# Kernel tuning notes

Measured on AMD Instinct MI355X. Metric: run time of the kernel, lower is better.

Reference implementation:

```python
import jax, jax.numpy as jnp
import numpy as np

NUM_SUBSET = 3
BN_EPS = 1e-5


def setup_inputs() -> dict:
    key = jax.random.key(0)
    ks = jax.random.split(key, 6)
    N, C, T, V = 32, 192, 256, 25
    x = jax.random.normal(ks[0], (N, C, T, V), dtype=jnp.float32)
    w_in = jax.random.normal(ks[1], (3 * C, C), dtype=jnp.float32) * (1.0 / np.sqrt(C))
    b_in = jax.random.normal(ks[2], (3 * C,), dtype=jnp.float32) * 0.02
    w_ff = jax.random.normal(ks[3], (C, C), dtype=jnp.float32) * (1.0 / np.sqrt(C))
    b_ff = jax.random.normal(ks[4], (C,), dtype=jnp.float32) * 0.02
    bn_gamma = jnp.ones((C,), dtype=jnp.float32)
    bn_beta = jnp.zeros((C,), dtype=jnp.float32)
    bn_mean = jnp.zeros((C,), dtype=jnp.float32)
    bn_var = jnp.ones((C,), dtype=jnp.float32)
    return dict(x=x, w_in=w_in, b_in=b_in, w_ff=w_ff, b_ff=b_ff,
                bn_gamma=bn_gamma, bn_beta=bn_beta, bn_mean=bn_mean, bn_var=bn_var)


def reference(x, w_in, b_in, w_ff, b_ff, bn_gamma, bn_beta, bn_mean, bn_var):
    N, C, T, V = x.shape
    S = NUM_SUBSET
    mid = C // S
    # 1x1 conv QKV projection: (N,C,T,V) x (3C,C) -> (N,3C,T,V)
    qkv = jnp.einsum('nctv,dc->ndtv', x, w_in) + b_in[None, :, None, None]
    qkv = qkv.reshape(N, 3 * S, mid, T, V)
    q, k, v = jnp.split(qkv, 3, axis=1)  # each (N,S,mid,T,V)
    # tanh-normalized attention over time: (N,S,T,T)
    att = jnp.tanh(jnp.einsum('nsctv,nscqv->nstq', q, k) / (mid * V))
    y = jnp.einsum('nstq,nscqv->nsctv', att, v).reshape(N, C, T, V)
    # ff_nett: 1x1 conv + BatchNorm (inference form)
    y = jnp.einsum('nctv,dc->ndtv', y, w_ff) + b_ff[None, :, None, None]
    inv = bn_gamma / jnp.sqrt(bn_var + BN_EPS)
    y = (y - bn_mean[None, :, None, None]) * inv[None, :, None, None] + bn_beta[None, :, None, None]
    # residual + LeakyReLU(0.1)
    z = x + y
    return jnp.where(z >= 0, z, 0.1 * z)
```

## Files before the change

kernel.cpp:

```cpp
#include <hip/hip_runtime.h>

#define TV 6400
#define NCH 192
#define D3 576

typedef unsigned short u16;
typedef unsigned int   u32;

typedef __attribute__((ext_vector_type(8))) short bf16x8;
typedef __attribute__((ext_vector_type(4))) float f32x4;

__device__ __forceinline__ float bf2f(u32 h) { return __uint_as_float(h << 16); }
__device__ __forceinline__ u16 f2bf(float f) {
    u32 u = __float_as_uint(f);
    return (u16)((u + 0x7FFFu + ((u >> 16) & 1u)) >> 16);
}

__global__ __launch_bounds__(256) void k_wcast(const float* __restrict__ w_in,
                                               const float* __restrict__ w_ff,
                                               u32* __restrict__ wb) {
    int i = blockIdx.x * 256 + threadIdx.x;
    float2 f;
    if (i < 55296) f = *(const float2*)(w_in + 2 * i);
    else           f = *(const float2*)(w_ff + 2 * (i - 55296));
    wb[i] = (u32)f2bf(f.x) | ((u32)f2bf(f.y) << 16);
}

__global__ __launch_bounds__(256) void k_qkv(const float* __restrict__ x,
                                             const u16* __restrict__ w_inb,
                                             const float* __restrict__ b_in,
                                             u16* __restrict__ qkv,
                                             u16* __restrict__ qt,
                                             u16* __restrict__ kt) {
    const int p0 = blockIdx.x * 128, n = blockIdx.y;
    const int tid = threadIdx.x;
    const int wid = tid >> 6, lane = tid & 63;
    const int wd = wid & 1, wp = wid >> 1;
    const int ml = lane & 15, kq = lane >> 4;

    __shared__ __align__(16) char Bs[128 * 384];
    __shared__ __align__(16) char As[64 * 384];
    float* L = (float*)As;

    for (int cc = 0; cc < 6; ++cc) {
        const float* xn = x + ((size_t)n * NCH + cc * 32) * TV + p0;
#pragma unroll
        for (int r = 0; r < 4; ++r) {
            int idx = tid + 256 * r;
            int c = idx >> 5, p4 = idx & 31;
            float4 v = *(const float4*)(xn + (size_t)c * TV + p4 * 4);
            *(float4*)&L[c * 129 + p4 * 4] = v;
        }
        __syncthreads();
        {
            int p = tid >> 1, half = tid & 1;
            u32 buf[8];
#pragma unroll
            for (int j = 0; j < 8; ++j) {
                float f0 = L[(half * 16 + 2 * j) * 129 + p];
                float f1 = L[(half * 16 + 2 * j + 1) * 129 + p];
                buf[j] = (u32)f2bf(f0) | ((u32)f2bf(f1) << 16);
            }
#pragma unroll
            for (int h = 0; h < 2; ++h) {
                int g = cc * 4 + half * 2 + h;
                uint4 u;
                u.x = buf[h * 4]; u.y = buf[h * 4 + 1];
                u.z = buf[h * 4 + 2]; u.w = buf[h * 4 + 3];
                *(uint4*)(Bs + p * 384 + (((g & ~7) | ((g ^ p) & 7)) << 4)) = u;
            }
        }
        __syncthreads();
    }

    for (int dt = 0; dt < 9; ++dt) {
#pragma unroll
        for (int r = 0; r < 6; ++r) {
            int idx = tid + 256 * r;
            int row = idx / 24, g = idx - row * 24;
            uint4 v = *(const uint4*)(w_inb + (size_t)(dt * 64 + row) * 192 + g * 8);
            *(uint4*)(As + row * 384 + (((g & ~7) | ((g ^ row) & 7)) << 4)) = v;
        }
        __syncthreads();

        bf16x8 aw[2][3][2];
#pragma unroll
        for (int mt = 0; mt < 2; ++mt) {
            int row = wd * 32 + mt * 16 + ml;
#pragma unroll
            for (int kk = 0; kk < 3; ++kk)
#pragma unroll
                for (int ks = 0; ks < 2; ++ks) {
                    int g = kk * 8 + ks * 4 + kq;
                    aw[mt][kk][ks] = *(const bf16x8*)(As + row * 384 + (((g & ~7) | ((g ^ row) & 7)) << 4));
                }
        }

        f32x4 acc[2][4];
#pragma unroll
        for (int i = 0; i < 2; i++)
#pragma unroll
            for (int j = 0; j < 4; j++)
#pragma unroll
                for (int r = 0; r < 4; r++) acc[i][j][r] = 0.f;

#pragma unroll
        for (int kk = 0; kk < 3; ++kk)
#pragma unroll
            for (int ks = 0; ks < 2; ++ks) {
                int g = kk * 8 + ks * 4 + kq;
                bf16x8 bx[4];
#pragma unroll
                for (int nt = 0; nt < 4; ++nt) {
                    int row = wp * 64 + nt * 16 + ml;
                    bx[nt] = *(const bf16x8*)(Bs + row * 384 + (((g & ~7) | ((g ^ row) & 7)) << 4));
                }
#pragma unroll
                for (int mt = 0; mt < 2; ++mt)
#pragma unroll
                    for (int nt = 0; nt < 4; ++nt)
                        acc[mt][nt] = __builtin_amdgcn_mfma_f32_16x16x32_bf16(aw[mt][kk][ks], bx[nt], acc[mt][nt], 0, 0, 0);
            }

        if (dt < 6) {
            const int s = (dt < 3) ? dt : dt - 3;
            u16* dstb = (dt < 3 ? qt : kt) + ((size_t)(n * 3 + s) * 6400 + p0) * 64;
#pragma unroll
            for (int mt = 0; mt < 2; ++mt) {
                int c = wd * 32 + mt * 16 + kq * 4;
                float4 bias = *(const float4*)(b_in + dt * 64 + c);
#pragma unroll
                for (int nt = 0; nt < 4; ++nt) {
                    int p = wp * 64 + nt * 16 + ml;
                    u32 w0 = (u32)f2bf(acc[mt][nt][0] + bias.x) | ((u32)f2bf(acc[mt][nt][1] + bias.y) << 16);
                    u32 w1 = (u32)f2bf(acc[mt][nt][2] + bias.z) | ((u32)f2bf(acc[mt][nt][3] + bias.w) << 16);
                    uint2 u; u.x = w0; u.y = w1;
                    *(uint2*)(dstb + (size_t)p * 64 + c) = u;
                }
            }
        } else {
#pragma unroll
            for (int mt = 0; mt < 2; ++mt) {
                int d = dt * 64 + wd * 32 + mt * 16 + kq * 4;
                float4 bias = *(const float4*)(b_in + d);
                u16* vdst = qkv + ((size_t)n * D3 + d) * TV;
#pragma unroll
                for (int nt = 0; nt < 4; ++nt) {
                    int p = p0 + wp * 64 + nt * 16 + ml;
                    vdst[(size_t)0 * TV + p] = f2bf(acc[mt][nt][0] + bias.x);
                    vdst[(size_t)1 * TV + p] = f2bf(acc[mt][nt][1] + bias.y);
                    vdst[(size_t)2 * TV + p] = f2bf(acc[mt][nt][2] + bias.z);
                    vdst[(size_t)3 * TV + p] = f2bf(acc[mt][nt][3] + bias.w);
                }
            }
        }
        __syncthreads();
    }
}

__global__ __launch_bounds__(256) void k_scores(const u16* __restrict__ qt,
                                                const u16* __restrict__ kt,
                                                u16* __restrict__ att) {
    const int b = blockIdx.z, t0 = blockIdx.y * 128, q0 = blockIdx.x * 128;
    const int tid = threadIdx.x;
    const int wid = tid >> 6, lane = tid & 63;
    const int wm = wid & 1, wn = wid >> 1;
    const int ml = lane & 15, kq = lane >> 4;

    __shared__ __align__(16) char As[128 * 128];
    __shared__ __align__(16) char Bs[128 * 128];

    f32x4 acc[4][4];
#pragma unroll
    for (int i = 0; i < 4; i++)
#pragma unroll
        for (int j = 0; j < 4; j++)
#pragma unroll
            for (int r = 0; r < 4; r++) acc[i][j][r] = 0.f;

    const u16* qb = qt + (size_t)b * 256 * 1600;
    const u16* kb = kt + (size_t)b * 256 * 1600;

    for (int kc = 0; kc < 1600; kc += 64) {
#pragma unroll
        for (int r = 0; r < 4; r++) {
            int idx = tid + 256 * r;
            int row = idx >> 3, g = idx & 7;
            uint4 v = *(const uint4*)(qb + (size_t)(t0 + row) * 1600 + kc + g * 8);
            *(uint4*)(As + row * 128 + (((g ^ row) & 7) << 4)) = v;
        }
#pragma unroll
        for (int r = 0; r < 4; r++) {
            int idx = tid + 256 * r;
            int row = idx >> 3, g = idx & 7;
            uint4 v = *(const uint4*)(kb + (size_t)(q0 + row) * 1600 + kc + g * 8);
            *(uint4*)(Bs + row * 128 + (((g ^ row) & 7) << 4)) = v;
        }
        __syncthreads();
#pragma unroll
        for (int ks = 0; ks < 2; ks++) {
            int gb = ks * 4 + kq;
            bf16x8 a[4], bb[4];
#pragma unroll
            for (int mt = 0; mt < 4; mt++) {
                int row = wm * 64 + mt * 16 + ml;
                a[mt] = *(const bf16x8*)(As + row * 128 + (((gb ^ row) & 7) << 4));
            }
#pragma unroll
            for (int nt = 0; nt < 4; nt++) {
                int row = wn * 64 + nt * 16 + ml;
                bb[nt] = *(const bf16x8*)(Bs + row * 128 + (((gb ^ row) & 7) << 4));
            }
#pragma unroll
            for (int mt = 0; mt < 4; mt++)
#pragma unroll
                for (int nt = 0; nt < 4; nt++)
                    acc[mt][nt] = __builtin_amdgcn_mfma_f32_16x16x32_bf16(a[mt], bb[nt], acc[mt][nt], 0, 0, 0);
        }
        __syncthreads();
    }

    const float sc = 1.0f / 1600.0f;
    u16* ab = att + (size_t)b * 65536;
#pragma unroll
    for (int mt = 0; mt < 4; mt++)
#pragma unroll
        for (int nt = 0; nt < 4; nt++) {
            int q = q0 + wn * 64 + nt * 16 + ml;
#pragma unroll
            for (int r = 0; r < 4; r++) {
                int t = t0 + wm * 64 + mt * 16 + kq * 4 + r;
                ab[(size_t)t * 256 + q] = f2bf(tanhf(acc[mt][nt][r] * sc));
            }
        }
}

__global__ __launch_bounds__(256) void k_trv(const u16* __restrict__ qkv,
                                             u16* __restrict__ vt) {
    const int q0 = blockIdx.x * 32;
    const int c0 = blockIdx.y * 32;
    const int b  = blockIdx.z;
    const int n = b / 3, s = b % 3;
    const int tid = threadIdx.x;

    __shared__ u16 L[32 * 800];

    const u16* src = qkv + ((size_t)n * D3 + 384 + s * 64 + c0) * TV + q0 * 25;
#pragma unroll
    for (int r = 0; r < 13; ++r) {
        int idx = tid + 256 * r;
        if (idx < 3200) {
            int c = idx / 100, w = idx - 100 * c;
            uint4 v = *(const uint4*)(src + (size_t)c * TV + w * 8);
            *(uint4*)&L[c * 800 + w * 8] = v;
        }
    }
    __syncthreads();

    u16* dst = vt + ((size_t)b * 1600 + c0) * 256 + q0;
#pragma unroll
    for (int r = 0; r < 4; ++r) {
        int idx = tid + 256 * r;
        if (idx < 800) {
            int c = idx / 25, v = idx - 25 * c;
            const u16* lp = &L[c * 800 + v];
            u32 buf[16];
#pragma unroll
            for (int j = 0; j < 16; ++j) {
                u32 lo = lp[(2 * j) * 25];
                u32 hi = lp[(2 * j + 1) * 25];
                buf[j] = lo | (hi << 16);
            }
            u16* dp = dst + (size_t)(v * 64 + c) * 256;
#pragma unroll
            for (int q4 = 0; q4 < 4; ++q4) {
                uint4 u; u.x = buf[q4 * 4]; u.y = buf[q4 * 4 + 1];
                u.z = buf[q4 * 4 + 2]; u.w = buf[q4 * 4 + 3];
                *(uint4*)(dp + q4 * 8) = u;
            }
        }
    }
}

__global__ __launch_bounds__(256) void k_av(const u16* __restrict__ att,
                                            const u16* __restrict__ vt,
                                            u16* __restrict__ y_t) {
    const int b = blockIdx.z, t0 = blockIdx.y * 128, cv0 = blockIdx.x * 128;
    const int n = b / 3, s = b % 3;
    const int tid = threadIdx.x;
    const int wid = tid >> 6, lane = tid & 63;
    const int wm = wid & 1, wn = wid >> 1;
    const int ml = lane & 15, kq = lane >> 4;

    __shared__ __align__(16) char As[128 * 128];
    __shared__ __align__(16) char Bs[128 * 128];

    f32x4 acc[4][4];
#pragma unroll
    for (int i = 0; i < 4; i++)
#pragma unroll
        for (int j = 0; j < 4; j++)
#pragma unroll
            for (int r = 0; r < 4; r++) acc[i][j][r] = 0.f;

    const u16* ab = att + (size_t)b * 65536;
    const u16* vb = vt + (size_t)b * 1600 * 256;

    for (int kc = 0; kc < 256; kc += 64) {
#pragma unroll
        for (int r = 0; r < 4; r++) {
            int idx = tid + 256 * r;
            int row = idx >> 3, g = idx & 7;
            uint4 u = *(const uint4*)(ab + (size_t)(t0 + row) * 256 + kc + g * 8);
            *(uint4*)(As + row * 128 + (((g ^ row) & 7) << 4)) = u;
        }
#pragma unroll
        for (int r = 0; r < 4; r++) {
            int idx = tid + 256 * r;
            int row = idx >> 3, g = idx & 7;
            int gr = cv0 + row; if (gr > 1599) gr = 1599;
            uint4 u = *(const uint4*)(vb + (size_t)gr * 256 + kc + g * 8);
            *(uint4*)(Bs + row * 128 + (((g ^ row) & 7) << 4)) = u;
        }
        __syncthreads();
#pragma unroll
        for (int ks = 0; ks < 2; ks++) {
            int gb = ks * 4 + kq;
            bf16x8 a[4], bb[4];
#pragma unroll
            for (int mt = 0; mt < 4; mt++) {
                int row = wm * 64 + mt * 16 + ml;
                a[mt] = *(const bf16x8*)(As + row * 128 + (((gb ^ row) & 7) << 4));
            }
#pragma unroll
            for (int nt = 0; nt < 4; nt++) {
                int row = wn * 64 + nt * 16 + ml;
                bb[nt] = *(const bf16x8*)(Bs + row * 128 + (((gb ^ row) & 7) << 4));
            }
#pragma unroll
            for (int mt = 0; mt < 4; mt++)
#pragma unroll
                for (int nt = 0; nt < 4; nt++)
                    acc[mt][nt] = __builtin_amdgcn_mfma_f32_16x16x32_bf16(a[mt], bb[nt], acc[mt][nt], 0, 0, 0);
        }
        __syncthreads();
    }

#pragma unroll
    for (int mt = 0; mt < 4; mt++)
#pragma unroll
        for (int nt = 0; nt < 4; nt++) {
            int cv = cv0 + wn * 64 + nt * 16 + ml;
            if (cv < 1600) {
                int v = cv >> 6, c = cv & 63;
                int cg = s * 64 + c;
#pragma unroll
                for (int r = 0; r < 4; r++) {
                    int t = t0 + wm * 64 + mt * 16 + kq * 4 + r;
                    y_t[((size_t)n * TV + t * 25 + v) * 192 + cg] = f2bf(acc[mt][nt][r]);
                }
            }
        }
}

__global__ __launch_bounds__(256) void k_ff(const u16* __restrict__ y_t,
                                            const float* __restrict__ x,
                                            const u16* __restrict__ w_ffb,
                                            const float* __restrict__ b_ff,
                                            const float* __restrict__ gamma,
                                            const float* __restrict__ beta,
                                            const float* __restrict__ mean,
                                            const float* __restrict__ var,
                                            float* __restrict__ out) {
    const int n = blockIdx.y, p0 = blockIdx.x * 128;
    const int tid = threadIdx.x;
    const int wid = tid >> 6, lane = tid & 63;
    const int wn = wid;
    const int ml = lane & 15, kq = lane >> 4;

    __shared__ __align__(16) char Aw[64 * 384];
    __shared__ __align__(16) char By[128 * 384];

#pragma unroll
    for (int r = 0; r < 12; ++r) {
        int idx = tid + 256 * r;
        int row = idx / 24, g = idx - row * 24;
        uint4 v = *(const uint4*)(y_t + ((size_t)n * TV + p0 + row) * 192 + g * 8);
        *(uint4*)(By + row * 384 + (((g & ~7) | ((g ^ row) & 7)) << 4)) = v;
    }

    for (int dt = 0; dt < 3; ++dt) {
#pragma unroll
        for (int r = 0; r < 6; ++r) {
            int idx = tid + 256 * r;
            int row = idx / 24, g = idx - row * 24;
            uint4 v = *(const uint4*)(w_ffb + (size_t)(dt * 64 + row) * 192 + g * 8);
            *(uint4*)(Aw + row * 384 + (((g & ~7) | ((g ^ row) & 7)) << 4)) = v;
        }
        __syncthreads();

        f32x4 acc[4][2];
#pragma unroll
        for (int i = 0; i < 4; i++)
#pragma unroll
            for (int j = 0; j < 2; j++)
#pragma unroll
                for (int r = 0; r < 4; r++) acc[i][j][r] = 0.f;

#pragma unroll
        for (int kk = 0; kk < 3; ++kk)
#pragma unroll
            for (int ks = 0; ks < 2; ++ks) {
                int g = kk * 8 + ks * 4 + kq;
                bf16x8 a[4], bb[2];
#pragma unroll
                for (int mt = 0; mt < 4; mt++) {
                    int row = mt * 16 + ml;
                    a[mt] = *(const bf16x8*)(Aw + row * 384 + (((g & ~7) | ((g ^ row) & 7)) << 4));
                }
#pragma unroll
                for (int nt = 0; nt < 2; nt++) {
                    int row = wn * 32 + nt * 16 + ml;
                    bb[nt] = *(const bf16x8*)(By + row * 384 + (((g & ~7) | ((g ^ row) & 7)) << 4));
                }
#pragma unroll
                for (int mt = 0; mt < 4; mt++)
#pragma unroll
                    for (int nt = 0; nt < 2; nt++)
                        acc[mt][nt] = __builtin_amdgcn_mfma_f32_16x16x32_bf16(a[mt], bb[nt], acc[mt][nt], 0, 0, 0);
            }

#pragma unroll
        for (int mt = 0; mt < 4; mt++)
#pragma unroll
            for (int r = 0; r < 4; r++) {
                int d = dt * 64 + mt * 16 + kq * 4 + r;
                float inv = gamma[d] * rsqrtf(var[d] + 1e-5f);
                float bias = b_ff[d], mu = mean[d], bt = beta[d];
#pragma unroll
                for (int nt = 0; nt < 2; nt++) {
                    int p = p0 + wn * 32 + nt * 16 + ml;
                    size_t xi = ((size_t)n * NCH + d) * TV + p;
                    float v = acc[mt][nt][r] + bias;
                    v = (v - mu) * inv + bt;
                    float z = x[xi] + v;
                    out[xi] = (z >= 0.f) ? z : 0.1f * z;
                }
            }
        __syncthreads();
    }
}

extern "C" void kernel_launch(void* const* d_in, const int* in_sizes, int n_in,
                              void* d_out, int out_size, void* d_ws, size_t ws_size,
                              hipStream_t stream) {
    const float* x     = (const float*)d_in[0];
    const float* w_in  = (const float*)d_in[1];
    const float* b_in  = (const float*)d_in[2];
    const float* w_ff  = (const float*)d_in[3];
    const float* b_ff  = (const float*)d_in[4];
    const float* gamma = (const float*)d_in[5];
    const float* beta  = (const float*)d_in[6];
    const float* mean  = (const float*)d_in[7];
    const float* var   = (const float*)d_in[8];

    u16* qkv = (u16*)d_ws;
    u16* att = (u16*)((char*)d_ws + 235929600ull);
    u16* y_t = (u16*)((char*)d_ws + 248512512ull);
    u32* wb  = (u32*)((char*)d_ws + 327155712ull);
    u16* w_inb = (u16*)wb;
    u16* w_ffb = w_inb + 110592;
    u16* qt = (u16*)d_out;
    u16* kt = qt + 39321600ull;
    u16* vt = qt;
    float* out = (float*)d_out;

    k_wcast <<<dim3(288),        dim3(256), 0, stream>>>(w_in, w_ff, wb);
    k_qkv   <<<dim3(50, 32),     dim3(256), 0, stream>>>(x, w_inb, b_in, qkv, qt, kt);
    k_scores<<<dim3(2, 2, 96),   dim3(256), 0, stream>>>(qt, kt, att);
    k_trv   <<<dim3(8, 2, 96),   dim3(256), 0, stream>>>(qkv, vt);
    k_av    <<<dim3(13, 2, 96),  dim3(256), 0, stream>>>(att, vt, y_t);
    k_ff    <<<dim3(50, 32),     dim3(256), 0, stream>>>(y_t, x, w_ffb, b_ff, gamma, beta, mean, var, out);
}
```

Measured before the change: 600.6 us.

## Register-prefetch next tiles in qkv/ff and shrink score/AV tiles for occupancy

```diff
diff --git a/kernel.cpp b/kernel.cpp
--- a/kernel.cpp
+++ b/kernel.cpp
@@ -42,16 +42,41 @@
     __shared__ __align__(16) char As[64 * 384];
     float* L = (float*)As;
 
+    uint4 wpre[6];
+#pragma unroll
+    for (int r = 0; r < 6; ++r) {
+        int idx = tid + 256 * r;
+        int row = idx / 24, g = idx - row * 24;
+        wpre[r] = *(const uint4*)(w_inb + (size_t)row * 192 + g * 8);
+    }
+
+    float4 pre[4];
+    {
+        const float* xn = x + (size_t)n * NCH * TV + p0;
+#pragma unroll
+        for (int r = 0; r < 4; ++r) {
+            int idx = tid + 256 * r;
+            int c = idx >> 5, p4 = idx & 31;
+            pre[r] = *(const float4*)(xn + (size_t)c * TV + p4 * 4);
+        }
+    }
     for (int cc = 0; cc < 6; ++cc) {
-        const float* xn = x + ((size_t)n * NCH + cc * 32) * TV + p0;
 #pragma unroll
         for (int r = 0; r < 4; ++r) {
             int idx = tid + 256 * r;
             int c = idx >> 5, p4 = idx & 31;
-            float4 v = *(const float4*)(xn + (size_t)c * TV + p4 * 4);
-            *(float4*)&L[c * 129 + p4 * 4] = v;
-        }
-        __syncthreads();
+            *(float4*)&L[c * 129 + p4 * 4] = pre[r];
+        }
+        __syncthreads();
+        if (cc < 5) {
+            const float* xn = x + ((size_t)n * NCH + (cc + 1) * 32) * TV + p0;
+#pragma unroll
+            for (int r = 0; r < 4; ++r) {
+                int idx = tid + 256 * r;
+                int c = idx >> 5, p4 = idx & 31;
+                pre[r] = *(const float4*)(xn + (size_t)c * TV + p4 * 4);
+            }
+        }
         {
             int p = tid >> 1, half = tid & 1;
             u32 buf[8];
@@ -78,10 +103,17 @@
         for (int r = 0; r < 6; ++r) {
             int idx = tid + 256 * r;
             int row = idx / 24, g = idx - row * 24;
-            uint4 v = *(const uint4*)(w_inb + (size_t)(dt * 64 + row) * 192 + g * 8);
-            *(uint4*)(As + row * 384 + (((g & ~7) | ((g ^ row) & 7)) << 4)) = v;
-        }
-        __syncthreads();
+            *(uint4*)(As + row * 384 + (((g & ~7) | ((g ^ row) & 7)) << 4)) = wpre[r];
+        }
+        __syncthreads();
+        if (dt < 8) {
+#pragma unroll
+            for (int r = 0; r < 6; ++r) {
+                int idx = tid + 256 * r;
+                int row = idx / 24, g = idx - row * 24;
+                wpre[r] = *(const uint4*)(w_inb + (size_t)((dt + 1) * 64 + row) * 192 + g * 8);
+            }
+        }
 
         bf16x8 aw[2][3][2];
 #pragma unroll
@@ -161,20 +193,20 @@
 __global__ __launch_bounds__(256) void k_scores(const u16* __restrict__ qt,
                                                 const u16* __restrict__ kt,
                                                 u16* __restrict__ att) {
-    const int b = blockIdx.z, t0 = blockIdx.y * 128, q0 = blockIdx.x * 128;
+    const int b = blockIdx.z, t0 = blockIdx.y * 64, q0 = blockIdx.x * 128;
     const int tid = threadIdx.x;
     const int wid = tid >> 6, lane = tid & 63;
-    const int wm = wid & 1, wn = wid >> 1;
+    const int wn = wid;
     const int ml = lane & 15, kq = lane >> 4;
 
-    __shared__ __align__(16) char As[128 * 128];
+    __shared__ __align__(16) char As[64 * 128];
     __shared__ __align__(16) char Bs[128 * 128];
 
-    f32x4 acc[4][4];
+    f32x4 acc[4][2];
 #pragma unroll
     for (int i = 0; i < 4; i++)
 #pragma unroll
-        for (int j = 0; j < 4; j++)
+        for (int j = 0; j < 2; j++)
 #pragma unroll
             for (int r = 0; r < 4; r++) acc[i][j][r] = 0.f;
 
@@ -183,7 +215,7 @@
 
     for (int kc = 0; kc < 1600; kc += 64) {
 #pragma unroll
-        for (int r = 0; r < 4; r++) {
+        for (int r = 0; r < 2; r++) {
             int idx = tid + 256 * r;
             int row = idx >> 3, g = idx & 7;
             uint4 v = *(const uint4*)(qb + (size_t)(t0 + row) * 1600 + kc + g * 8);
@@ -200,21 +232,21 @@
 #pragma unroll
         for (int ks = 0; ks < 2; ks++) {
             int gb = ks * 4 + kq;
-            bf16x8 a[4], bb[4];
+            bf16x8 a[4], bb[2];
 #pragma unroll
             for (int mt = 0; mt < 4; mt++) {
-                int row = wm * 64 + mt * 16 + ml;
+                int row = mt * 16 + ml;
                 a[mt] = *(const bf16x8*)(As + row * 128 + (((gb ^ row) & 7) << 4));
             }
 #pragma unroll
-            for (int nt = 0; nt < 4; nt++) {
-                int row = wn * 64 + nt * 16 + ml;
+            for (int nt = 0; nt < 2; nt++) {
+                int row = wn * 32 + nt * 16 + ml;
                 bb[nt] = *(const bf16x8*)(Bs + row * 128 + (((gb ^ row) & 7) << 4));
             }
 #pragma unroll
             for (int mt = 0; mt < 4; mt++)
 #pragma unroll
-                for (int nt = 0; nt < 4; nt++)
+                for (int nt = 0; nt < 2; nt++)
                     acc[mt][nt] = __builtin_amdgcn_mfma_f32_16x16x32_bf16(a[mt], bb[nt], acc[mt][nt], 0, 0, 0);
         }
         __syncthreads();
@@ -225,11 +257,11 @@
 #pragma unroll
     for (int mt = 0; mt < 4; mt++)
 #pragma unroll
-        for (int nt = 0; nt < 4; nt++) {
-            int q = q0 + wn * 64 + nt * 16 + ml;
+        for (int nt = 0; nt < 2; nt++) {
+            int q = q0 + wn * 32 + nt * 16 + ml;
 #pragma unroll
             for (int r = 0; r < 4; r++) {
-                int t = t0 + wm * 64 + mt * 16 + kq * 4 + r;
+                int t = t0 + mt * 16 + kq * 4 + r;
                 ab[(size_t)t * 256 + q] = f2bf(tanhf(acc[mt][nt][r] * sc));
             }
         }
@@ -285,7 +317,7 @@
 __global__ __launch_bounds__(256) void k_av(const u16* __restrict__ att,
                                             const u16* __restrict__ vt,
                                             u16* __restrict__ y_t) {
-    const int b = blockIdx.z, t0 = blockIdx.y * 128, cv0 = blockIdx.x * 128;
+    const int b = blockIdx.z, t0 = blockIdx.y * 128, v = blockIdx.x;
     const int n = b / 3, s = b % 3;
     const int tid = threadIdx.x;
     const int wid = tid >> 6, lane = tid & 63;
@@ -293,18 +325,18 @@
     const int ml = lane & 15, kq = lane >> 4;
 
     __shared__ __align__(16) char As[128 * 128];
-    __shared__ __align__(16) char Bs[128 * 128];
-
-    f32x4 acc[4][4];
+    __shared__ __align__(16) char Bs[64 * 128];
+
+    f32x4 acc[4][2];
 #pragma unroll
     for (int i = 0; i < 4; i++)
 #pragma unroll
-        for (int j = 0; j < 4; j++)
+        for (int j = 0; j < 2; j++)
 #pragma unroll
             for (int r = 0; r < 4; r++) acc[i][j][r] = 0.f;
 
     const u16* ab = att + (size_t)b * 65536;
-    const u16* vb = vt + (size_t)b * 1600 * 256;
+    const u16* vb = vt + ((size_t)b * 1600 + v * 64) * 256;
 
     for (int kc = 0; kc < 256; kc += 64) {
 #pragma unroll
@@ -315,32 +347,31 @@
             *(uint4*)(As + row * 128 + (((g ^ row) & 7) << 4)) = u;
         }
 #pragma unroll
-        for (int r = 0; r < 4; r++) {
+        for (int r = 0; r < 2; r++) {
             int idx = tid + 256 * r;
             int row = idx >> 3, g = idx & 7;
-            int gr = cv0 + row; if (gr > 1599) gr = 1599;
-            uint4 u = *(const uint4*)(vb + (size_t)gr * 256 + kc + g * 8);
+            uint4 u = *(const uint4*)(vb + (size_t)row * 256 + kc + g * 8);
             *(uint4*)(Bs + row * 128 + (((g ^ row) & 7) << 4)) = u;
         }
         __syncthreads();
 #pragma unroll
         for (int ks = 0; ks < 2; ks++) {
             int gb = ks * 4 + kq;
-            bf16x8 a[4], bb[4];
+            bf16x8 a[4], bb[2];
 #pragma unroll
             for (int mt = 0; mt < 4; mt++) {
                 int row = wm * 64 + mt * 16 + ml;
                 a[mt] = *(const bf16x8*)(As + row * 128 + (((gb ^ row) & 7) << 4));
             }
 #pragma unroll
-            for (int nt = 0; nt < 4; nt++) {
-                int row = wn * 64 + nt * 16 + ml;
+            for (int nt = 0; nt < 2; nt++) {
+                int row = wn * 32 + nt * 16 + ml;
                 bb[nt] = *(const bf16x8*)(Bs + row * 128 + (((gb ^ row) & 7) << 4));
             }
 #pragma unroll
             for (int mt = 0; mt < 4; mt++)
 #pragma unroll
-                for (int nt = 0; nt < 4; nt++)
+                for (int nt = 0; nt < 2; nt++)
                     acc[mt][nt] = __builtin_amdgcn_mfma_f32_16x16x32_bf16(a[mt], bb[nt], acc[mt][nt], 0, 0, 0);
         }
         __syncthreads();
@@ -349,16 +380,12 @@
 #pragma unroll
     for (int mt = 0; mt < 4; mt++)
 #pragma unroll
-        for (int nt = 0; nt < 4; nt++) {
-            int cv = cv0 + wn * 64 + nt * 16 + ml;
-            if (cv < 1600) {
-                int v = cv >> 6, c = cv & 63;
-                int cg = s * 64 + c;
-#pragma unroll
-                for (int r = 0; r < 4; r++) {
-                    int t = t0 + wm * 64 + mt * 16 + kq * 4 + r;
-                    y_t[((size_t)n * TV + t * 25 + v) * 192 + cg] = f2bf(acc[mt][nt][r]);
-                }
+        for (int nt = 0; nt < 2; nt++) {
+            int cg = s * 64 + wn * 32 + nt * 16 + ml;
+#pragma unroll
+            for (int r = 0; r < 4; r++) {
+                int t = t0 + wm * 64 + mt * 16 + kq * 4 + r;
+                y_t[((size_t)n * TV + t * 25 + v) * 192 + cg] = f2bf(acc[mt][nt][r]);
             }
         }
 }
@@ -389,15 +416,30 @@
         *(uint4*)(By + row * 384 + (((g & ~7) | ((g ^ row) & 7)) << 4)) = v;
     }
 
+    uint4 awp[6];
+#pragma unroll
+    for (int r = 0; r < 6; ++r) {
+        int idx = tid + 256 * r;
+        int row = idx / 24, g = idx - row * 24;
+        awp[r] = *(const uint4*)(w_ffb + (size_t)row * 192 + g * 8);
+    }
+
     for (int dt = 0; dt < 3; ++dt) {
 #pragma unroll
         for (int r = 0; r < 6; ++r) {
             int idx = tid + 256 * r;
             int row = idx / 24, g = idx - row * 24;
-            uint4 v = *(const uint4*)(w_ffb + (size_t)(dt * 64 + row) * 192 + g * 8);
-            *(uint4*)(Aw + row * 384 + (((g & ~7) | ((g ^ row) & 7)) << 4)) = v;
-        }
-        __syncthreads();
+            *(uint4*)(Aw + row * 384 + (((g & ~7) | ((g ^ row) & 7)) << 4)) = awp[r];
+        }
+        __syncthreads();
+        if (dt < 2) {
+#pragma unroll
+            for (int r = 0; r < 6; ++r) {
+                int idx = tid + 256 * r;
+                int row = idx / 24, g = idx - row * 24;
+                awp[r] = *(const uint4*)(w_ffb + (size_t)((dt + 1) * 64 + row) * 192 + g * 8);
+            }
+        }
 
         f32x4 acc[4][2];
 #pragma unroll
@@ -477,8 +519,8 @@
 
     k_wcast <<<dim3(288),        dim3(256), 0, stream>>>(w_in, w_ff, wb);
     k_qkv   <<<dim3(50, 32),     dim3(256), 0, stream>>>(x, w_inb, b_in, qkv, qt, kt);
-    k_scores<<<dim3(2, 2, 96),   dim3(256), 0, stream>>>(qt, kt, att);
+    k_scores<<<dim3(2, 4, 96),   dim3(256), 0, stream>>>(qt, kt, att);
     k_trv   <<<dim3(8, 2, 96),   dim3(256), 0, stream>>>(qkv, vt);
-    k_av    <<<dim3(13, 2, 96),  dim3(256), 0, stream>>>(att, vt, y_t);
+    k_av    <<<dim3(25, 2, 96),  dim3(256), 0, stream>>>(att, vt, y_t);
     k_ff    <<<dim3(50, 32),     dim3(256), 0, stream>>>(y_t, x, w_ffb, b_ff, gamma, beta, mean, var, out);
 }
```

After: 732.7 us. 22.0% more time.
